# Kernel tuning notes

Hardware: AMD Instinct MI355X
Metric: run time of the kernel (lower is better)

## Reference

```python
import jax, jax.numpy as jnp
import numpy as np

B, R, P, DP, DR, N, RK = 4, 256, 64, 384, 512, 48, 24


def _ln(x, w, b, eps=1e-5):
    m = x.mean(-1, keepdims=True)
    v = ((x - m) ** 2).mean(-1, keepdims=True)
    return (x - m) / jnp.sqrt(v + eps) * w + b


def _l2norm(x, eps=1e-6):
    return x / jnp.maximum(jnp.linalg.norm(x, axis=-1, keepdims=True), eps)


def setup_inputs() -> dict:
    key = jax.random.key(0)
    ks = jax.random.split(key, 16)
    s = 0.02
    rnd = lambda k, shp: jax.random.normal(k, shp, jnp.float32) * s
    inp = {
        'patch_tokens': jax.random.normal(ks[0], (B, R, P, DP), jnp.float32),
        'patch_mask': jax.random.randint(ks[1], (B, R, P), 0, 2) > 0,
        'near_mask': jax.random.randint(ks[2], (R, R), 0, 2) > 0,
        'far_mask': jax.random.randint(ks[3], (R, R), 0, 2) > 0,
        'local_pos': rnd(ks[4], (1, 1, P, DP)),
        'gate_ln_w': jnp.ones(DP), 'gate_ln_b': jnp.zeros(DP),
        'gate_w1': rnd(ks[5], (DP, DR)), 'gate_b1': jnp.zeros(DR),
        'gate_w2': rnd(ks[6], (DR, 1)), 'gate_b2': jnp.zeros(1),
        'proj_ln1_w': jnp.ones(DP), 'proj_ln1_b': jnp.zeros(DP),
        'proj_w1': rnd(ks[7], (DP, DR)), 'proj_b1': jnp.zeros(DR),
        'proj_w2': rnd(ks[8], (DR, DR)), 'proj_b2': jnp.zeros(DR),
        'proj_ln2_w': jnp.ones(DR), 'proj_ln2_b': jnp.zeros(DR),
        'in_proj_w': rnd(ks[9], (DR, 2 * DR)),
        'x_proj_w': rnd(ks[10], (DR, RK + 2 * N)),
        'dt_w': rnd(ks[11], (RK, DR)),
        'dt_b': jax.random.uniform(ks[12], (DR,), jnp.float32, -4.0, -2.0),
        'A_log': jnp.tile(jnp.log(jnp.arange(1, N + 1, dtype=jnp.float32))[None, :], (DR, 1)),
        'D_param': jnp.ones(DR),
        'out_proj_w': rnd(ks[13], (DR, DR)),
        'scan_ln_w': jnp.ones(DR), 'scan_ln_b': jnp.zeros(DR),
    }
    return inp


def _forward(patch_tokens, patch_mask, near_mask, far_mask, local_pos,
             gate_ln_w, gate_ln_b, gate_w1, gate_b1, gate_w2, gate_b2,
             proj_ln1_w, proj_ln1_b, proj_w1, proj_b1, proj_w2, proj_b2,
             proj_ln2_w, proj_ln2_b, in_proj_w, x_proj_w, dt_w, dt_b,
             A_log, D_param, out_proj_w, scan_ln_w, scan_ln_b):
    # ---- GatedRegionAggregator ----
    x = patch_tokens + local_pos  # [B,R,P,DP]
    g = _ln(x, gate_ln_w, gate_ln_b)
    g = jax.nn.gelu(g @ gate_w1 + gate_b1, approximate=False)
    logits = (g @ gate_w2 + gate_b2)[..., 0]  # [B,R,P]
    logits = jnp.where(patch_mask, logits, jnp.finfo(logits.dtype).min)
    attn = jax.nn.softmax(logits, axis=-1) * patch_mask
    attn = attn / jnp.maximum(attn.sum(-1, keepdims=True), 1e-6)
    pooled = jnp.einsum('brp,brpd->brd', attn, x)  # [B,R,DP]
    p = _ln(pooled, proj_ln1_w, proj_ln1_b)
    p = jax.nn.gelu(p @ proj_w1 + proj_b1, approximate=False)
    p = _ln(p @ proj_w2 + proj_b2, proj_ln2_w, proj_ln2_b)
    p = jnp.nan_to_num(p, nan=0.0, posinf=1.0, neginf=-1.0)
    region = _l2norm(p)  # [B,R,DR]

    # ---- SlowSelectiveScan1D over region sequence (L = R) ----
    xz = region @ in_proj_w  # [B,L,2*DR]
    u, z = jnp.split(xz, 2, axis=-1)
    prm = u @ x_proj_w  # [B,L,RK+2N]
    dt_raw, Bm, Cm = prm[..., :RK], prm[..., RK:RK + N], prm[..., RK + N:]
    delta = jnp.minimum(jax.nn.softplus(dt_raw @ dt_w + dt_b), 10.0)  # [B,L,DR]
    A = -jnp.minimum(jnp.exp(A_log), 1e4)  # [DR,N]
    dA = jnp.exp(jnp.clip(delta[..., None] * A[None, None], -30.0, 30.0))  # [B,L,DR,N]
    dBu = delta[..., None] * Bm[:, :, None, :] * u[..., None]  # [B,L,DR,N]
    log_cumA = jnp.cumsum(jnp.log(jnp.maximum(dA, 1e-38)), axis=1)
    h = jnp.exp(log_cumA) * jnp.cumsum(dBu * jnp.exp(-log_cumA), axis=1)
    y_seq = jnp.einsum('bln,bldn->bld', Cm, h) + D_param * u
    y = (y_seq * jax.nn.silu(z)) @ out_proj_w
    out = _ln(region + jnp.nan_to_num(y, nan=0.0, posinf=1.0, neginf=-1.0),
              scan_ln_w, scan_ln_b)  # [B,R,DR]

    # ---- topology_loss_static ----
    rt = _l2norm(out.astype(jnp.float32))
    sim = jnp.einsum('brd,bsd->brs', rt, rt)  # [B,R,R]
    near = near_mask.astype(sim.dtype)[None]
    far = far_mask.astype(sim.dtype)[None]
    near_loss = ((1.0 - sim) * near).sum() / jnp.maximum(near.sum(), 1.0)
    far_loss = (jax.nn.relu(sim - 0.2) * far).sum() / jnp.maximum(far.sum(), 1.0)
    return out, near_loss + far_loss


def reference(patch_tokens, patch_mask, near_mask, far_mask, local_pos,
              gate_ln_w, gate_ln_b, gate_w1, gate_b1, gate_w2, gate_b2,
              proj_ln1_w, proj_ln1_b, proj_w1, proj_b1, proj_w2, proj_b2,
              proj_ln2_w, proj_ln2_b, in_proj_w, x_proj_w, dt_w, dt_b,
              A_log, D_param, out_proj_w, scan_ln_w, scan_ln_b):
    return _forward(patch_tokens, patch_mask, near_mask, far_mask, local_pos,
                    gate_ln_w, gate_ln_b, gate_w1, gate_b1, gate_w2, gate_b2,
                    proj_ln1_w, proj_ln1_b, proj_w1, proj_b1, proj_w2, proj_b2,
                    proj_ln2_w, proj_ln2_b, in_proj_w, x_proj_w, dt_w, dt_b,
                    A_log, D_param, out_proj_w, scan_ln_w, scan_ln_b)
```

## Files before the change

kernel.cpp:

```cpp
#include <hip/hip_runtime.h>
#include <hip/hip_bf16.h>
#include <math.h>

#define B_ 4
#define R_ 256
#define P_ 64
#define DP_ 384
#define DR_ 512
#define N_ 48
#define RK_ 24
#define MROWS (B_*R_*P_)
#define REGS  (B_*R_)

typedef unsigned short ushort_t;
typedef __attribute__((ext_vector_type(8))) short bf16x8;
typedef __attribute__((ext_vector_type(4))) float f32x4;

#define GLOAD16(g, l) __builtin_amdgcn_global_load_lds( \
    (const __attribute__((address_space(1))) unsigned int*)(g), \
    (__attribute__((address_space(3))) unsigned int*)(l), 16, 0, 0)

#define OFF_PW1  0
#define OFF_PW2  196608
#define OFF_INPW 458752
#define OFF_XPW  983040
#define OFF_DTW  1044480
#define NW_TOT   1056768

__device__ __forceinline__ float us2f(unsigned short u){
  union { unsigned int i; float f; } x; x.i = ((unsigned int)u) << 16; return x.f;
}
__device__ __forceinline__ unsigned short f2us(float f){
  __hip_bfloat16 h = __float2bfloat16(f);
  return *reinterpret_cast<unsigned short*>(&h);
}
__device__ __forceinline__ float gelu_f(float x){
  return 0.5f * x * (1.0f + erff(x * 0.70710678118654752f));
}
__device__ __forceinline__ float wred_sum(float v){
#pragma unroll
  for (int m = 1; m < 64; m <<= 1) v += __shfl_xor(v, m, 64);
  return v;
}
__device__ __forceinline__ void block_sum4(float v[4], float* s){
  int lane = threadIdx.x & 63, wid = threadIdx.x >> 6;
#pragma unroll
  for (int i = 0; i < 4; ++i){
    float x = v[i];
#pragma unroll
    for (int m = 1; m < 64; m <<= 1) x += __shfl_xor(x, m, 64);
    if (lane == 0) s[wid * 4 + i] = x;
  }
  __syncthreads();
  if (threadIdx.x < 4){
    float t = 0.f;
    for (int t2 = 0; t2 < 8; ++t2) t += s[t2 * 4 + threadIdx.x];
    s[32 + threadIdx.x] = t;
  }
  __syncthreads();
#pragma unroll
  for (int i = 0; i < 4; ++i) v[i] = s[32 + i];
  __syncthreads();
}
__device__ __forceinline__ void block_sum2(float& a, float& b, float* s){
  int lane = threadIdx.x & 63, wid = threadIdx.x >> 6;
  float x = a, y = b;
#pragma unroll
  for (int m = 1; m < 64; m <<= 1){ x += __shfl_xor(x, m, 64); y += __shfl_xor(y, m, 64); }
  if (lane == 0){ s[wid * 2] = x; s[wid * 2 + 1] = y; }
  __syncthreads();
  if (threadIdx.x < 2){
    float t = 0.f;
    for (int j = 0; j < 8; ++j) t += s[j * 2 + threadIdx.x];
    s[16 + threadIdx.x] = t;
  }
  __syncthreads();
  a = s[16]; b = s[17];
  __syncthreads();
}

__global__ __launch_bounds__(512) void k_prep(
    const float* __restrict__ gw1, const float* __restrict__ glnw,
    const float* __restrict__ glnb, const float* __restrict__ gb1,
    ushort_t* __restrict__ W1pT, float* __restrict__ s1,
    float* __restrict__ b1p, float* __restrict__ accum){
  __shared__ float pss[8][64], psb[8][64];
  int tid = threadIdx.x, seg = tid >> 6, nl = tid & 63;
  int n = blockIdx.x * 64 + nl;
  if (blockIdx.x == 0 && tid < 4) accum[tid] = 0.f;
  float s = 0.f, sb = 0.f;
  int k0 = seg * 48;
  for (int i = 0; i < 48; ++i){
    int k = k0 + i;
    float w1 = gw1[k * DR_ + n];
    float v = glnw[k] * w1;
    unsigned short vr = f2us(v);
    s  += us2f(vr);
    sb += glnb[k] * w1;
    W1pT[(size_t)n * DP_ + k] = vr;
  }
  pss[seg][nl] = s; psb[seg][nl] = sb;
  __syncthreads();
  if (tid < 64){
    float ts = 0.f, tb = 0.f;
    for (int j = 0; j < 8; ++j){ ts += pss[j][tid]; tb += psb[j][tid]; }
    s1[blockIdx.x * 64 + tid] = ts;
    b1p[blockIdx.x * 64 + tid] = gb1[blockIdx.x * 64 + tid] + tb;
  }
}

__global__ __launch_bounds__(512) void k_cast(
    const float* __restrict__ pw1, const float* __restrict__ pw2,
    const float* __restrict__ inpw, const float* __restrict__ xpw,
    const float* __restrict__ dtw, ushort_t* __restrict__ dst){
  int i = (blockIdx.x * 512 + threadIdx.x) * 4;
  if (i >= NW_TOT) return;
  const float* s; int off;
  if (i < OFF_PW2){ s = pw1; off = OFF_PW1; }
  else if (i < OFF_INPW){ s = pw2; off = OFF_PW2; }
  else if (i < OFF_XPW){ s = inpw; off = OFF_INPW; }
  else if (i < OFF_DTW){ s = xpw; off = OFF_XPW; }
  else { s = dtw; off = OFF_DTW; }
  float4 v = *(const float4*)(s + (i - off));
  ushort_t* d = dst + i;
  d[0] = f2us(v.x); d[1] = f2us(v.y); d[2] = f2us(v.z); d[3] = f2us(v.w);
}

__global__ __launch_bounds__(512) void k_xform(
    const float* __restrict__ pt, const float* __restrict__ lp,
    ushort_t* __restrict__ xb, float* __restrict__ mu, float* __restrict__ rsg){
  int tid = threadIdx.x, w = tid >> 6, lane = tid & 63;
  size_t r = (size_t)blockIdx.x * 8 + w;
  int p = (int)(r & (P_ - 1));
  const float* xr = pt + r * DP_ + lane * 6;
  const float* lr = lp + (size_t)p * DP_ + lane * 6;
  float x[6];
  float s = 0.f, ss = 0.f;
#pragma unroll
  for (int i = 0; i < 6; i += 2){
    float2 a = *(const float2*)(xr + i);
    float2 b = *(const float2*)(lr + i);
    x[i] = a.x + b.x; x[i + 1] = a.y + b.y;
  }
#pragma unroll
  for (int i = 0; i < 6; ++i){ s += x[i]; ss += x[i] * x[i]; }
  s = wred_sum(s); ss = wred_sum(ss);
  if (lane == 0){
    float m = s * (1.f / DP_);
    float var = ss * (1.f / DP_) - m * m;
    mu[r] = m;
    rsg[r] = rsqrtf(var + 1e-5f);
  }
  ushort_t* xw = xb + r * DP_ + lane * 6;
#pragma unroll
  for (int i = 0; i < 6; i += 2){
    ushort2 u2; u2.x = f2us(x[i]); u2.y = f2us(x[i + 1]);
    *(ushort2*)(xw + i) = u2;
  }
}

__global__ __launch_bounds__(512, 2) void k_gate(
    const ushort_t* __restrict__ xb,
    const ushort_t* __restrict__ BT,
    const float* __restrict__ mu, const float* __restrict__ rsg,
    const float* __restrict__ s1, const float* __restrict__ b1p,
    const float* __restrict__ w2, float* __restrict__ logits){
  __shared__ __align__(16) ushort_t Abuf[6][64 * 64];
  __shared__ float logit_lds[64];
  __shared__ float smu[64], srs[64];
  int tid = threadIdx.x;
  int lane = tid & 63, w = tid >> 6;
  int t = lane & 15, g = lane >> 4;
  long r0 = (long)blockIdx.x * 64;
  if (tid < 64){
    logit_lds[tid] = 0.f;
    smu[tid] = mu[r0 + tid];
    srs[tid] = rsg[r0 + tid];
  }

  f32x4 acc[4][4];
#pragma unroll
  for (int m = 0; m < 4; ++m)
#pragma unroll
    for (int n = 0; n < 4; ++n) acc[m][n] = (f32x4){0.f, 0.f, 0.f, 0.f};

  int arow8 = (w << 3) + (lane >> 3);
  int akc = lane & 7;
  const ushort_t* asrc0 = xb + (size_t)(r0 + arow8) * DP_ + ((akc ^ (arow8 & 7)) << 3);
#pragma unroll
  for (int kt = 0; kt < 6; ++kt)
    GLOAD16(asrc0 + kt * 64, Abuf[kt] + (w << 9));
  __syncthreads();

#pragma unroll
  for (int kt = 0; kt < 6; ++kt){
    bf16x8 bfr[2][4];
#pragma unroll
    for (int kk = 0; kk < 2; ++kk)
#pragma unroll
      for (int n = 0; n < 4; ++n){
        int rowb = w * 64 + n * 16 + t;
        bfr[kk][n] = *(const bf16x8*)(BT + (size_t)rowb * DP_ + kt * 64 + (kk * 4 + g) * 8);
      }
#pragma unroll
    for (int kk = 0; kk < 2; ++kk){
      int ch = kk * 4 + g;
      bf16x8 af[4];
#pragma unroll
      for (int m = 0; m < 4; ++m){
        int row = m * 16 + t;
        af[m] = *(const bf16x8*)(Abuf[kt] + row * 64 + ((ch ^ (row & 7)) << 3));
      }
#pragma unroll
      for (int m = 0; m < 4; ++m)
#pragma unroll
        for (int n = 0; n < 4; ++n)
          acc[m][n] = __builtin_amdgcn_mfma_f32_16x16x32_bf16(af[m], bfr[kk][n], acc[m][n], 0, 0, 0);
    }
  }

  float w2c[4], s1c[4], b1c[4];
#pragma unroll
  for (int n = 0; n < 4; ++n){
    int c = w * 64 + n * 16 + t;
    w2c[n] = w2[c]; s1c[n] = s1[c]; b1c[n] = b1p[c];
  }
#pragma unroll
  for (int m = 0; m < 4; ++m){
#pragma unroll
    for (int j = 0; j < 4; ++j){
      int rl = m * 16 + g * 4 + j;
      float mur = smu[rl], rs = srs[rl];
      float part = 0.f;
#pragma unroll
      for (int n = 0; n < 4; ++n){
        float gp = rs * acc[m][n][j] - mur * rs * s1c[n] + b1c[n];
        part += gelu_f(gp) * w2c[n];
      }
#pragma unroll
      for (int msk = 1; msk < 16; msk <<= 1) part += __shfl_xor(part, msk, 64);
      if (t == 0) atomicAdd(&logit_lds[rl], part);
    }
  }
  __syncthreads();
  if (tid < 64) logits[r0 + tid] = logit_lds[tid];
}

__global__ __launch_bounds__(512) void k_pool(
    const ushort_t* __restrict__ xb, const float* __restrict__ logits,
    const int* __restrict__ pmask, float* __restrict__ pooled){
  __shared__ float attn[64];
  __shared__ float part[8][DP_];
  int tid = threadIdx.x;
  long r0 = (long)blockIdx.x * 64;
  if (tid < 64){
    int mk = pmask[r0 + tid];
    float lv = logits[r0 + tid];
    float lm = mk ? lv : -3.4e38f;
    float M = lm;
#pragma unroll
    for (int m2 = 1; m2 < 64; m2 <<= 1) M = fmaxf(M, __shfl_xor(M, m2, 64));
    float e = mk ? __expf(lv - M) : 0.f;
    float S = e;
#pragma unroll
    for (int m2 = 1; m2 < 64; m2 <<= 1) S += __shfl_xor(S, m2, 64);
    float a = (S > 0.f) ? e / S : 0.f;
    float S2 = a;
#pragma unroll
    for (int m2 = 1; m2 < 64; m2 <<= 1) S2 += __shfl_xor(S2, m2, 64);
    attn[tid] = a / fmaxf(S2, 1e-6f);
  }
  __syncthreads();
  if (tid < 384){
    int pg = tid / 48, c = tid % 48;
    float acc[8] = {0,0,0,0,0,0,0,0};
#pragma unroll
    for (int i = 0; i < 8; ++i){
      int p = pg + i * 8;
      bf16x8 v = *(const bf16x8*)(xb + (size_t)(r0 + p) * DP_ + c * 8);
      float ap = attn[p];
#pragma unroll
      for (int j = 0; j < 8; ++j) acc[j] = fmaf(ap, us2f((unsigned short)v[j]), acc[j]);
    }
#pragma unroll
    for (int j = 0; j < 8; ++j) part[pg][c * 8 + j] = acc[j];
  }
  __syncthreads();
  if (tid < DP_){
    float s = 0.f;
#pragma unroll
    for (int g2 = 0; g2 < 8; ++g2) s += part[g2][tid];
    pooled[(long)blockIdx.x * DP_ + tid] = s;
  }
}

__global__ __launch_bounds__(512, 4) void k_region(
    const float* __restrict__ pooled,
    const float* __restrict__ ln1w, const float* __restrict__ ln1b,
    const ushort_t* __restrict__ wblob, const float* __restrict__ pb1,
    const float* __restrict__ pb2,
    const float* __restrict__ ln2w, const float* __restrict__ ln2b,
    const float* __restrict__ dtb,
    float* __restrict__ region, float* __restrict__ uT, float* __restrict__ zT,
    float* __restrict__ deltaT, float* __restrict__ BmT, float* __restrict__ CmT){
  const ushort_t* pw1b  = wblob + OFF_PW1;
  const ushort_t* pw2b  = wblob + OFF_PW2;
  const ushort_t* inpwb = wblob + OFF_INPW;
  const ushort_t* xpwb  = wblob + OFF_XPW;
  const ushort_t* dtwb  = wblob + OFF_DTW;
  __shared__ float xr[2][DP_];
  __shared__ float p1[2][DR_];
  __shared__ float rg[2][DR_];
  __shared__ float us[2][DR_];
  __shared__ float ps[4][2][128];
  __shared__ float prm[2][RK_ + 2 * N_];
  __shared__ float red[24];
  int tid = threadIdx.x;
  int r0 = blockIdx.x * 2;
  for (int i = tid; i < 2 * DP_; i += 512) xr[i / DP_][i % DP_] = pooled[(long)r0 * DP_ + i];
  __syncthreads();
  float v0 = (tid < DP_) ? xr[0][tid] : 0.f;
  float v1 = (tid < DP_) ? xr[1][tid] : 0.f;
  float s0 = v0, s1v = v1;
  block_sum2(s0, s1v, red);
  float dv0 = (tid < DP_) ? (v0 - s0 * (1.f / DP_)) : 0.f;
  float dv1 = (tid < DP_) ? (v1 - s1v * (1.f / DP_)) : 0.f;
  float q0 = dv0 * dv0, q1 = dv1 * dv1;
  block_sum2(q0, q1, red);
  if (tid < DP_){
    float lw = ln1w[tid], lb = ln1b[tid];
    xr[0][tid] = dv0 * rsqrtf(q0 * (1.f / DP_) + 1e-5f) * lw + lb;
    xr[1][tid] = dv1 * rsqrtf(q1 * (1.f / DP_) + 1e-5f) * lw + lb;
  }
  __syncthreads();
  {
    float pb = pb1[tid];
    float a0 = pb, a1 = pb;
    for (int k0 = 0; k0 < DP_; k0 += 16){
      ushort_t wv[16];
#pragma unroll
      for (int j = 0; j < 16; ++j) wv[j] = pw1b[(k0 + j) * DR_ + tid];
#pragma unroll
      for (int j = 0; j < 16; ++j){
        float wf = us2f(wv[j]);
        a0 = fmaf(xr[0][k0 + j], wf, a0);
        a1 = fmaf(xr[1][k0 + j], wf, a1);
      }
    }
    p1[0][tid] = gelu_f(a0); p1[1][tid] = gelu_f(a1);
  }
  __syncthreads();
  float qq0, qq1;
  {
    float pb = pb2[tid];
    float a0 = pb, a1 = pb;
    for (int k0 = 0; k0 < DR_; k0 += 16){
      ushort_t wv[16];
#pragma unroll
      for (int j = 0; j < 16; ++j) wv[j] = pw2b[(k0 + j) * DR_ + tid];
#pragma unroll
      for (int j = 0; j < 16; ++j){
        float wf = us2f(wv[j]);
        a0 = fmaf(p1[0][k0 + j], wf, a0);
        a1 = fmaf(p1[1][k0 + j], wf, a1);
      }
    }
    qq0 = a0; qq1 = a1;
  }
  {
    float m0 = qq0, m1 = qq1;
    block_sum2(m0, m1, red);
    float d0 = qq0 - m0 * (1.f / DR_), d1 = qq1 - m1 * (1.f / DR_);
    float w0 = d0 * d0, w1 = d1 * d1;
    block_sum2(w0, w1, red);
    float lw = ln2w[tid], lb = ln2b[tid];
    float o0 = d0 * rsqrtf(w0 * (1.f / DR_) + 1e-5f) * lw + lb;
    float o1 = d1 * rsqrtf(w1 * (1.f / DR_) + 1e-5f) * lw + lb;
    if (isnan(o0)) o0 = 0.f; else if (isinf(o0)) o0 = (o0 > 0.f) ? 1.f : -1.f;
    if (isnan(o1)) o1 = 0.f; else if (isinf(o1)) o1 = (o1 > 0.f) ? 1.f : -1.f;
    float n0 = o0 * o0, n1 = o1 * o1;
    block_sum2(n0, n1, red);
    float r0v = o0 / fmaxf(sqrtf(n0), 1e-6f);
    float r1v = o1 / fmaxf(sqrtf(n1), 1e-6f);
    rg[0][tid] = r0v; rg[1][tid] = r1v;
    region[(long)r0 * DR_ + tid] = r0v;
    region[(long)(r0 + 1) * DR_ + tid] = r1v;
  }
  __syncthreads();
  {
    float ua0 = 0.f, ua1 = 0.f, zb0 = 0.f, zb1 = 0.f;
    for (int k0 = 0; k0 < DR_; k0 += 8){
      ushort_t w1v[8], w2v[8];
#pragma unroll
      for (int j = 0; j < 8; ++j){
        w1v[j] = inpwb[(k0 + j) * 1024 + tid];
        w2v[j] = inpwb[(k0 + j) * 1024 + tid + 512];
      }
#pragma unroll
      for (int j = 0; j < 8; ++j){
        float x0 = rg[0][k0 + j], x1 = rg[1][k0 + j];
        float wa = us2f(w1v[j]), wb = us2f(w2v[j]);
        ua0 = fmaf(x0, wa, ua0); ua1 = fmaf(x1, wa, ua1);
        zb0 = fmaf(x0, wb, zb0); zb1 = fmaf(x1, wb, zb1);
      }
    }
    us[0][tid] = ua0; us[1][tid] = ua1;
    uT[(long)tid * REGS + r0] = ua0;
    uT[(long)tid * REGS + r0 + 1] = ua1;
    zT[(long)tid * REGS + r0] = zb0;
    zT[(long)tid * REGS + r0 + 1] = zb1;
  }
  __syncthreads();
  {
    int sseg = tid >> 7, c = tid & 127;
    float pr0 = 0.f, pr1 = 0.f;
    if (c < RK_ + 2 * N_){
      int kb = sseg * 128;
      for (int k0 = kb; k0 < kb + 128; k0 += 16){
        ushort_t wv[16];
#pragma unroll
        for (int j = 0; j < 16; ++j) wv[j] = xpwb[(k0 + j) * (RK_ + 2 * N_) + c];
#pragma unroll
        for (int j = 0; j < 16; ++j){
          float wf = us2f(wv[j]);
          pr0 = fmaf(us[0][k0 + j], wf, pr0);
          pr1 = fmaf(us[1][k0 + j], wf, pr1);
        }
      }
    }
    ps[sseg][0][c] = pr0; ps[sseg][1][c] = pr1;
  }
  __syncthreads();
  if (tid < 256){
    int rr2 = tid >> 7, cc = tid & 127;
    if (cc < RK_ + 2 * N_)
      prm[rr2][cc] = ps[0][rr2][cc] + ps[1][rr2][cc] + ps[2][rr2][cc] + ps[3][rr2][cc];
  }
  __syncthreads();
#pragma unroll
  for (int r = 0; r < 2; ++r){
    float aa = dtb[tid];
#pragma unroll
    for (int j = 0; j < RK_; ++j) aa = fmaf(prm[r][j], us2f(dtwb[j * DR_ + tid]), aa);
    float sp = (aa > 20.f) ? aa : log1pf(expf(aa));
    deltaT[(long)tid * REGS + r0 + r] = fminf(sp, 10.f);
  }
  if (tid < N_){
#pragma unroll
    for (int r = 0; r < 2; ++r){
      BmT[(long)tid * REGS + r0 + r] = prm[r][RK_ + tid];
      CmT[(long)tid * REGS + r0 + r] = prm[r][RK_ + N_ + tid];
    }
  }
}

__global__ __launch_bounds__(256) void k_scan(
    const float* __restrict__ deltaT, const float* __restrict__ uT,
    const float* __restrict__ zT, const float* __restrict__ BmT,
    const float* __restrict__ CmT, const float* __restrict__ alog,
    const float* __restrict__ Dp, float* __restrict__ ys){
  __shared__ float sAn[N_];
  __shared__ float sA[N_][4];
  __shared__ float sB[N_][4];
  int tid = threadIdx.x, lane = tid & 63, w = tid >> 6;
  int ch = blockIdx.x;
  int b = ch >> 9, d = ch & (DR_ - 1);
  if (tid < N_) sAn[tid] = -fminf(__expf(alog[d * N_ + tid]), 10000.f);
  long col = (long)b * R_ + tid;
  float dl = deltaT[(long)d * REGS + col];
  float uu = uT[(long)d * REGS + col];
  float zz = zT[(long)d * REGS + col];
  float Dd = Dp[d];
  float part = 0.f;
  __syncthreads();
  for (int nc = 0; nc < 6; ++nc){
    float bmv[8], cmv[8];
#pragma unroll
    for (int j = 0; j < 8; ++j){
      bmv[j] = BmT[(long)(nc * 8 + j) * REGS + col];
      cmv[j] = CmT[(long)(nc * 8 + j) * REGS + col];
    }
    float aA[8], aB[8];
#pragma unroll
    for (int j = 0; j < 8; ++j){
      int n = nc * 8 + j;
      float cc = fminf(fmaxf(dl * sAn[n], -30.f), 30.f);
      float a = exp2f(cc * 1.44269504f);
      float bv = dl * bmv[j] * uu;
#pragma unroll
      for (int s = 1; s < 64; s <<= 1){
        float a_sh = __shfl_up(a, (unsigned)s, 64);
        float b_sh = __shfl_up(bv, (unsigned)s, 64);
        float nb = fmaf(a, b_sh, bv);
        float na = a * a_sh;
        if (lane >= s){ bv = nb; a = na; }
      }
      aA[j] = a; aB[j] = bv;
      if (lane == 63){ sA[n][w] = a; sB[n][w] = bv; }
    }
    __syncthreads();
#pragma unroll
    for (int j = 0; j < 8; ++j){
      int n = nc * 8 + j;
      float hin = 0.f;
#pragma unroll
      for (int tt = 0; tt < 3; ++tt){
        if (tt < w) hin = sA[n][tt] * hin + sB[n][tt];
      }
      float h = fmaf(aA[j], hin, aB[j]);
      part = fmaf(cmv[j], h, part);
    }
    if (nc < 5) __syncthreads();
  }
  float yv = part + Dd * uu;
  float sz = zz / (1.f + __expf(-zz));
  ys[col * DR_ + d] = yv * sz;
}

__global__ __launch_bounds__(512) void k_out(
    const float* __restrict__ ys, const float* __restrict__ W,
    const float* __restrict__ region, const float* __restrict__ lnw,
    const float* __restrict__ lnb, float* __restrict__ outp,
    float* __restrict__ rt){
  __shared__ float yr[4][DR_];
  __shared__ float red[40];
  int tid = threadIdx.x;
  int r0 = blockIdx.x * 4;
  for (int i = tid; i < 4 * DR_; i += 512) yr[i >> 9][i & 511] = ys[(long)r0 * DR_ + i];
  __syncthreads();
  float y[4] = {0,0,0,0};
  for (int k0 = 0; k0 < DR_; k0 += 8){
    float wv[8];
#pragma unroll
    for (int j = 0; j < 8; ++j) wv[j] = W[(k0 + j) * DR_ + tid];
#pragma unroll
    for (int j = 0; j < 8; ++j){
#pragma unroll
      for (int i = 0; i < 4; ++i) y[i] = fmaf(yr[i][k0 + j], wv[j], y[i]);
    }
  }
  float v[4], t4[4];
#pragma unroll
  for (int i = 0; i < 4; ++i){
    if (isnan(y[i])) y[i] = 0.f; else if (isinf(y[i])) y[i] = (y[i] > 0.f) ? 1.f : -1.f;
    v[i] = region[(long)(r0 + i) * DR_ + tid] + y[i];
    t4[i] = v[i];
  }
  block_sum4(t4, red);
  float dv[4];
#pragma unroll
  for (int i = 0; i < 4; ++i){ dv[i] = v[i] - t4[i] * (1.f / DR_); t4[i] = dv[i] * dv[i]; }
  block_sum4(t4, red);
  float o[4];
  float lw = lnw[tid], lb = lnb[tid];
#pragma unroll
  for (int i = 0; i < 4; ++i){
    o[i] = dv[i] * rsqrtf(t4[i] * (1.f / DR_) + 1e-5f) * lw + lb;
    outp[(long)(r0 + i) * DR_ + tid] = o[i];
    t4[i] = o[i] * o[i];
  }
  block_sum4(t4, red);
#pragma unroll
  for (int i = 0; i < 4; ++i)
    rt[(long)(r0 + i) * DR_ + tid] = o[i] / fmaxf(sqrtf(t4[i]), 1e-6f);
}

__global__ __launch_bounds__(512) void k_loss(
    const float* __restrict__ rt, const int* __restrict__ nearm,
    const int* __restrict__ farm, float* __restrict__ accum){
  __shared__ __align__(16) float ar[4][DR_];
  __shared__ float ps[2][4][256];
  __shared__ float wsum[8][4];
  int blk = blockIdx.x, tid = threadIdx.x;
  int b = blk >> 6, q0 = (blk & 63) * 4;
  const float* rtb = rt + (long)b * R_ * DR_;
  for (int i = tid; i < 4 * DR_; i += 512) ar[i >> 9][i & 511] = rtb[(long)q0 * DR_ + i];
  __syncthreads();
  int s = tid & 255, h = tid >> 8;
  const float* rsrow = rtb + (long)s * DR_ + h * 256;
  float dq[4] = {0.f, 0.f, 0.f, 0.f};
  for (int k = 0; k < 256; k += 4){
    float4 yv = *(const float4*)(rsrow + k);
#pragma unroll
    for (int q = 0; q < 4; ++q){
      float4 x = *(const float4*)(&ar[q][h * 256 + k]);
      dq[q] += x.x * yv.x + x.y * yv.y + x.z * yv.z + x.w * yv.w;
    }
  }
#pragma unroll
  for (int q = 0; q < 4; ++q) ps[h][q][s] = dq[q];
  __syncthreads();
  float nl = 0.f, fl = 0.f, nc = 0.f, fc = 0.f;
  if (tid < 256){
#pragma unroll
    for (int q = 0; q < 4; ++q){
      float dot = ps[0][q][tid] + ps[1][q][tid];
      int nm = nearm[(q0 + q) * R_ + tid], fm = farm[(q0 + q) * R_ + tid];
      if (nm){ nl += 1.f - dot; if (b == 0) nc += 1.f; }
      if (fm){ fl += fmaxf(dot - 0.2f, 0.f); if (b == 0) fc += 1.f; }
    }
  }
  nl = wred_sum(nl); fl = wred_sum(fl); nc = wred_sum(nc); fc = wred_sum(fc);
  int w = tid >> 6, lane = tid & 63;
  if (lane == 0){ wsum[w][0] = nl; wsum[w][1] = fl; wsum[w][2] = nc; wsum[w][3] = fc; }
  __syncthreads();
  if (tid == 0){
    float a0 = 0, a1 = 0, a2 = 0, a3 = 0;
    for (int i = 0; i < 8; i++){ a0 += wsum[i][0]; a1 += wsum[i][1]; a2 += wsum[i][2]; a3 += wsum[i][3]; }
    atomicAdd(&accum[0], a0); atomicAdd(&accum[1], a1);
    if (b == 0){ atomicAdd(&accum[2], a2); atomicAdd(&accum[3], a3); }
  }
}

__global__ void k_final(const float* __restrict__ accum, float* __restrict__ outp){
  if (threadIdx.x == 0){
    float loss = accum[0] / fmaxf(accum[2], 1.f) + accum[1] / fmaxf(accum[3], 1.f);
    outp[REGS * DR_] = loss;
  }
}

extern "C" void kernel_launch(void* const* d_in, const int* in_sizes, int n_in,
                              void* d_out, int out_size, void* d_ws, size_t ws_size,
                              hipStream_t stream){
  const float* pt    = (const float*)d_in[0];
  const int*   pmask = (const int*)d_in[1];
  const int*   nearm = (const int*)d_in[2];
  const int*   farm  = (const int*)d_in[3];
  const float* lp    = (const float*)d_in[4];
  const float* glnw  = (const float*)d_in[5];
  const float* glnb  = (const float*)d_in[6];
  const float* gw1   = (const float*)d_in[7];
  const float* gb1   = (const float*)d_in[8];
  const float* gw2   = (const float*)d_in[9];
  const float* pln1w = (const float*)d_in[11];
  const float* pln1b = (const float*)d_in[12];
  const float* pw1   = (const float*)d_in[13];
  const float* pb1   = (const float*)d_in[14];
  const float* pw2   = (const float*)d_in[15];
  const float* pb2   = (const float*)d_in[16];
  const float* pln2w = (const float*)d_in[17];
  const float* pln2b = (const float*)d_in[18];
  const float* inpw  = (const float*)d_in[19];
  const float* xpw   = (const float*)d_in[20];
  const float* dtw   = (const float*)d_in[21];
  const float* dtb   = (const float*)d_in[22];
  const float* alog  = (const float*)d_in[23];
  const float* dpar  = (const float*)d_in[24];
  const float* opw   = (const float*)d_in[25];
  const float* slnw  = (const float*)d_in[26];
  const float* slnb  = (const float*)d_in[27];

  char* ws = (char*)d_ws;
  size_t off = 0;
  auto alloc = [&](size_t bytes){ size_t o = off; off += (bytes + 255) & ~(size_t)255; return o; };
  ushort_t* W1pT  = (ushort_t*)(ws + alloc((size_t)DR_ * DP_ * 2));
  float* s1     = (float*)(ws + alloc(DR_ * 4));
  float* b1p    = (float*)(ws + alloc(DR_ * 4));
  ushort_t* wblob = (ushort_t*)(ws + alloc((size_t)NW_TOT * 2));
  ushort_t* xb  = (ushort_t*)(ws + alloc((size_t)MROWS * DP_ * 2));
  float* mu     = (float*)(ws + alloc((size_t)MROWS * 4));
  float* rsg    = (float*)(ws + alloc((size_t)MROWS * 4));
  float* logits = (float*)(ws + alloc((size_t)MROWS * 4));
  float* pooled = (float*)(ws + alloc((size_t)REGS * DP_ * 4));
  float* region = (float*)(ws + alloc((size_t)REGS * DR_ * 4));
  float* uT     = (float*)(ws + alloc((size_t)REGS * DR_ * 4));
  float* zT     = (float*)(ws + alloc((size_t)REGS * DR_ * 4));
  float* deltaT = (float*)(ws + alloc((size_t)REGS * DR_ * 4));
  float* BmT    = (float*)(ws + alloc((size_t)REGS * N_ * 4));
  float* CmT    = (float*)(ws + alloc((size_t)REGS * N_ * 4));
  float* ys     = (float*)(ws + alloc((size_t)REGS * DR_ * 4));
  float* rt     = (float*)(ws + alloc((size_t)REGS * DR_ * 4));
  float* accum  = (float*)(ws + alloc(4 * 4));

  float* outp = (float*)d_out;

  k_prep<<<dim3(8), dim3(512), 0, stream>>>(gw1, glnw, glnb, gb1, W1pT, s1, b1p, accum);
  k_cast<<<dim3((NW_TOT / 4 + 511) / 512), dim3(512), 0, stream>>>(pw1, pw2, inpw, xpw, dtw, wblob);
  k_xform<<<dim3(MROWS / 8), dim3(512), 0, stream>>>(pt, lp, xb, mu, rsg);
  k_gate<<<dim3(REGS), dim3(512), 0, stream>>>(xb, W1pT, mu, rsg, s1, b1p, gw2, logits);
  k_pool<<<dim3(REGS), dim3(512), 0, stream>>>(xb, logits, pmask, pooled);
  k_region<<<dim3(REGS / 2), dim3(512), 0, stream>>>(pooled, pln1w, pln1b, wblob, pb1, pb2, pln2w, pln2b,
                                                     dtb, region, uT, zT, deltaT, BmT, CmT);
  k_scan<<<dim3(B_ * DR_), dim3(256), 0, stream>>>(deltaT, uT, zT, BmT, CmT, alog, dpar, ys);
  k_out<<<dim3(REGS / 4), dim3(512), 0, stream>>>(ys, opw, region, slnw, slnb, outp, rt);
  k_loss<<<dim3(REGS / 4), dim3(512), 0, stream>>>(rt, nearm, farm, accum);
  k_final<<<dim3(1), dim3(64), 0, stream>>>(accum, outp);
}
```

Before: 335.7 us.

## Retile gate GEMM to 128-row blocks with double-buffered A and cheaper GELU

The gate kernel now processes 128 patch rows per block with 1024 threads. Each of the 16 waves computes a 32-column slice across all 128 rows, so every B (weight) fragment load is reused over twice as many rows. The A tile is double-buffered in LDS across the K loop instead of being loaded whole up front, which cuts LDS use and overlaps loads with MFMA. GELU's erff is replaced by the Abramowitz-Stegun polynomial erf approximation, which lowers ALU cost but adds a small approximation error of roughly 1e-7 absolute.

```diff
diff --git a/kernel.cpp b/kernel.cpp
--- a/kernel.cpp
+++ b/kernel.cpp
@@ -35,7 +35,14 @@
   return *reinterpret_cast<unsigned short*>(&h);
 }
 __device__ __forceinline__ float gelu_f(float x){
-  return 0.5f * x * (1.0f + erff(x * 0.70710678118654752f));
+  float u = x * 0.70710678118654752f;
+  float au = fabsf(u);
+  float tt = 1.0f / fmaf(0.3275911f, au, 1.0f);
+  float poly = tt * fmaf(tt, fmaf(tt, fmaf(tt, fmaf(tt, 1.061405429f, -1.453152027f),
+                       1.421413741f), -0.284496736f), 0.254829592f);
+  float erfv = 1.0f - poly * __expf(-au * au);
+  erfv = (u < 0.f) ? -erfv : erfv;
+  return 0.5f * x * (1.0f + erfv);
 }
 __device__ __forceinline__ float wred_sum(float v){
 #pragma unroll
@@ -159,81 +166,79 @@
   }
 }
 
-__global__ __launch_bounds__(512, 2) void k_gate(
+__global__ __launch_bounds__(1024) void k_gate(
     const ushort_t* __restrict__ xb,
     const ushort_t* __restrict__ BT,
     const float* __restrict__ mu, const float* __restrict__ rsg,
     const float* __restrict__ s1, const float* __restrict__ b1p,
     const float* __restrict__ w2, float* __restrict__ logits){
-  __shared__ __align__(16) ushort_t Abuf[6][64 * 64];
-  __shared__ float logit_lds[64];
-  __shared__ float smu[64], srs[64];
+  __shared__ __align__(16) ushort_t Abuf[2][128 * 64];
+  __shared__ float logit_lds[128];
+  __shared__ float smu[128], srs[128];
   int tid = threadIdx.x;
   int lane = tid & 63, w = tid >> 6;
   int t = lane & 15, g = lane >> 4;
-  long r0 = (long)blockIdx.x * 64;
-  if (tid < 64){
+  long r0 = (long)blockIdx.x * 128;
+  if (tid < 128){
     logit_lds[tid] = 0.f;
     smu[tid] = mu[r0 + tid];
     srs[tid] = rsg[r0 + tid];
   }
 
-  f32x4 acc[4][4];
-#pragma unroll
-  for (int m = 0; m < 4; ++m)
-#pragma unroll
-    for (int n = 0; n < 4; ++n) acc[m][n] = (f32x4){0.f, 0.f, 0.f, 0.f};
-
-  int arow8 = (w << 3) + (lane >> 3);
-  int akc = lane & 7;
-  const ushort_t* asrc0 = xb + (size_t)(r0 + arow8) * DP_ + ((akc ^ (arow8 & 7)) << 3);
-#pragma unroll
-  for (int kt = 0; kt < 6; ++kt)
-    GLOAD16(asrc0 + kt * 64, Abuf[kt] + (w << 9));
-  __syncthreads();
-
-#pragma unroll
+  f32x4 acc[8][2];
+#pragma unroll
+  for (int m = 0; m < 8; ++m)
+#pragma unroll
+    for (int n = 0; n < 2; ++n) acc[m][n] = (f32x4){0.f, 0.f, 0.f, 0.f};
+
+  int ro = lane >> 3, c = lane & 7;
+  int srow = (w << 3) + ro;
+  const ushort_t* asrc = xb + (size_t)(r0 + srow) * DP_ + ((c ^ (srow & 7)) << 3);
+
+  GLOAD16(asrc, Abuf[0] + (w << 9));
+  __syncthreads();
+
   for (int kt = 0; kt < 6; ++kt){
-    bf16x8 bfr[2][4];
+    int cb = kt & 1;
+    if (kt < 5) GLOAD16(asrc + (kt + 1) * 64, Abuf[cb ^ 1] + (w << 9));
+    bf16x8 bfr[2][2];
 #pragma unroll
     for (int kk = 0; kk < 2; ++kk)
 #pragma unroll
-      for (int n = 0; n < 4; ++n){
-        int rowb = w * 64 + n * 16 + t;
-        bfr[kk][n] = *(const bf16x8*)(BT + (size_t)rowb * DP_ + kt * 64 + (kk * 4 + g) * 8);
+      for (int n = 0; n < 2; ++n){
+        int col = w * 32 + n * 16 + t;
+        bfr[kk][n] = *(const bf16x8*)(BT + (size_t)col * DP_ + kt * 64 + (kk * 4 + g) * 8);
       }
 #pragma unroll
     for (int kk = 0; kk < 2; ++kk){
       int ch = kk * 4 + g;
-      bf16x8 af[4];
-#pragma unroll
-      for (int m = 0; m < 4; ++m){
+#pragma unroll
+      for (int m = 0; m < 8; ++m){
         int row = m * 16 + t;
-        af[m] = *(const bf16x8*)(Abuf[kt] + row * 64 + ((ch ^ (row & 7)) << 3));
-      }
-#pragma unroll
-      for (int m = 0; m < 4; ++m)
-#pragma unroll
-        for (int n = 0; n < 4; ++n)
-          acc[m][n] = __builtin_amdgcn_mfma_f32_16x16x32_bf16(af[m], bfr[kk][n], acc[m][n], 0, 0, 0);
-    }
-  }
-
-  float w2c[4], s1c[4], b1c[4];
-#pragma unroll
-  for (int n = 0; n < 4; ++n){
-    int c = w * 64 + n * 16 + t;
-    w2c[n] = w2[c]; s1c[n] = s1[c]; b1c[n] = b1p[c];
-  }
-#pragma unroll
-  for (int m = 0; m < 4; ++m){
+        bf16x8 af = *(const bf16x8*)(Abuf[cb] + row * 64 + ((ch ^ (row & 7)) << 3));
+#pragma unroll
+        for (int n = 0; n < 2; ++n)
+          acc[m][n] = __builtin_amdgcn_mfma_f32_16x16x32_bf16(af, bfr[kk][n], acc[m][n], 0, 0, 0);
+      }
+    }
+    __syncthreads();
+  }
+
+  float w2c[2], s1c[2], b1c[2];
+#pragma unroll
+  for (int n = 0; n < 2; ++n){
+    int col = w * 32 + n * 16 + t;
+    w2c[n] = w2[col]; s1c[n] = s1[col]; b1c[n] = b1p[col];
+  }
+#pragma unroll
+  for (int m = 0; m < 8; ++m){
 #pragma unroll
     for (int j = 0; j < 4; ++j){
       int rl = m * 16 + g * 4 + j;
       float mur = smu[rl], rs = srs[rl];
       float part = 0.f;
 #pragma unroll
-      for (int n = 0; n < 4; ++n){
+      for (int n = 0; n < 2; ++n){
         float gp = rs * acc[m][n][j] - mur * rs * s1c[n] + b1c[n];
         part += gelu_f(gp) * w2c[n];
       }
@@ -243,7 +248,7 @@
     }
   }
   __syncthreads();
-  if (tid < 64) logits[r0 + tid] = logit_lds[tid];
+  if (tid < 128) logits[r0 + tid] = logit_lds[tid];
 }
 
 __global__ __launch_bounds__(512) void k_pool(
@@ -677,7 +682,7 @@
   k_prep<<<dim3(8), dim3(512), 0, stream>>>(gw1, glnw, glnb, gb1, W1pT, s1, b1p, accum);
   k_cast<<<dim3((NW_TOT / 4 + 511) / 512), dim3(512), 0, stream>>>(pw1, pw2, inpw, xpw, dtw, wblob);
   k_xform<<<dim3(MROWS / 8), dim3(512), 0, stream>>>(pt, lp, xb, mu, rsg);
-  k_gate<<<dim3(REGS), dim3(512), 0, stream>>>(xb, W1pT, mu, rsg, s1, b1p, gw2, logits);
+  k_gate<<<dim3(MROWS / 128), dim3(1024), 0, stream>>>(xb, W1pT, mu, rsg, s1, b1p, gw2, logits);
   k_pool<<<dim3(REGS), dim3(512), 0, stream>>>(xb, logits, pmask, pooled);
   k_region<<<dim3(REGS / 2), dim3(512), 0, stream>>>(pooled, pln1w, pln1b, wblob, pb1, pb2, pln2w, pln2b,
                                                      dtb, region, uT, zT, deltaT, BmT, CmT);
```

Measured after the change: 322.8 us. -3.8%, faster.
